# Optimization experiments

Measured on AMD Instinct MI355X. Metric: run time of the kernel, lower is better.

The kernel has to match this reference:

```python
import jax, jax.numpy as jnp
import numpy as np

N_HEAD = 32
N_KV_HEAD = 8
HEAD_DIM = 64
ROPE_THETA = 10000.0


def apply_rope(x):
    # x: [B, H, T, D], interleaved-pair RoPE (rotary_embedding_torch style)
    B, H, T, D = x.shape
    inv_freq = 1.0 / (ROPE_THETA ** (jnp.arange(0, D, 2, dtype=jnp.float32) / D))  # [D/2]
    ang = jnp.arange(T, dtype=jnp.float32)[:, None] * inv_freq[None, :]  # [T, D/2]
    cos = jnp.cos(ang)[None, None].astype(x.dtype)  # [1,1,T,D/2]
    sin = jnp.sin(ang)[None, None].astype(x.dtype)
    xe = x[..., 0::2]
    xo = x[..., 1::2]
    re = xe * cos - xo * sin
    ro = xo * cos + xe * sin
    return jnp.stack([re, ro], axis=-1).reshape(B, H, T, D)


def setup_inputs() -> dict:
    key = jax.random.key(0)
    ks = jax.random.split(key, 5)
    B, T, C = 2, 2048, 2048
    kv_dim = N_KV_HEAD * HEAD_DIM
    s = 0.02
    return {
        "x": jax.random.normal(ks[0], (B, T, C), jnp.float32),
        "wq": jax.random.normal(ks[1], (C, C), jnp.float32) * s,
        "wk": jax.random.normal(ks[2], (C, kv_dim), jnp.float32) * s,
        "wv": jax.random.normal(ks[3], (C, kv_dim), jnp.float32) * s,
        "wo": jax.random.normal(ks[4], (C, C), jnp.float32) * s,
    }


def reference(x, wq, wk, wv, wo):
    B, T, C = x.shape
    hd = HEAD_DIM
    q = (x @ wq).reshape(B, T, N_HEAD, hd).transpose(0, 2, 1, 3)      # [B,H,T,d]
    k = (x @ wk).reshape(B, T, N_KV_HEAD, hd).transpose(0, 2, 1, 3)   # [B,Hkv,T,d]
    v = (x @ wv).reshape(B, T, N_KV_HEAD, hd).transpose(0, 2, 1, 3)
    q = apply_rope(q)
    k = apply_rope(k)
    rep = N_HEAD // N_KV_HEAD
    k = jnp.repeat(k, rep, axis=1)  # repeat_interleave over head dim
    v = jnp.repeat(v, rep, axis=1)
    att = jnp.einsum('bhqd,bhkd->bhqk', q, k) * (1.0 / np.sqrt(hd))
    causal = jnp.tril(jnp.ones((T, T), dtype=bool))
    att = jnp.where(causal[None, None], att, jnp.finfo(att.dtype).min)
    att = jax.nn.softmax(att, axis=-1)
    y = jnp.einsum('bhqk,bhkd->bhqd', att, v)
    y = y.transpose(0, 2, 1, 3).reshape(B, T, C)
    return y @ wo
```

## Files before the change

kernel.cpp:

```cpp
#include <hip/hip_runtime.h>
#include <hip/hip_bf16.h>
#include <cstdint>
#include <cstddef>


using bf16 = __hip_bfloat16;
using f32x4  = __attribute__((ext_vector_type(4))) float;
using f32x16 = __attribute__((ext_vector_type(16))) float;
using short8 = __attribute__((ext_vector_type(8))) short;
using u32x4  = __attribute__((ext_vector_type(4))) unsigned int;

typedef __attribute__((address_space(1))) const void* gp1_t;
typedef __attribute__((address_space(3))) void*       lp3_t;

#define GLOAD_LDS16(g, l)                                                     \
  __builtin_amdgcn_global_load_lds((gp1_t)(const void*)(g), (lp3_t)(void*)(l), 16, 0, 0)

#define MFMA16(a, b, c) __builtin_amdgcn_mfma_f32_16x16x32_bf16(a, b, c, 0, 0, 0)
#define MFMA32(a, b, c) __builtin_amdgcn_mfma_f32_32x32x16_bf16(a, b, c, 0, 0, 0)

static constexpr int Bd  = 2;
static constexpr int Td  = 2048;
static constexpr int Cd  = 2048;
static constexpr int NH  = 32;
static constexpr int NKV = 8;
static constexpr int HD  = 64;
static constexpr int Md  = Bd * Td;

__device__ inline float bf2f(unsigned short u) {
  union { unsigned int i; float f; } v; v.i = ((unsigned int)u) << 16; return v.f;
}
__device__ inline unsigned short f2bfbits(float f) {
  union { float f; unsigned int u; } v; v.f = f;
  unsigned int r = v.u + 0x7fffu + ((v.u >> 16) & 1u);
  return (unsigned short)(r >> 16);
}
__device__ inline unsigned int pkbf(float a, float b) {
  unsigned int r;
  asm("v_cvt_pk_bf16_f32 %0, %1, %2" : "=v"(r) : "v"(a), "v"(b));
  return r;
}
__device__ inline void plswapf(float& a, float& b) {
  asm("v_permlane32_swap_b32 %0, %1" : "+v"(a), "+v"(b));
}
__device__ inline void plswapu(unsigned int& a, unsigned int& b) {
  asm("v_permlane32_swap_b32 %0, %1" : "+v"(a), "+v"(b));
}
__device__ inline float hmax16(const f32x16& v) {
  float a0 = fmaxf(v[0], v[1]),   a1 = fmaxf(v[2], v[3]);
  float a2 = fmaxf(v[4], v[5]),   a3 = fmaxf(v[6], v[7]);
  float a4 = fmaxf(v[8], v[9]),   a5 = fmaxf(v[10], v[11]);
  float a6 = fmaxf(v[12], v[13]), a7 = fmaxf(v[14], v[15]);
  float b0 = fmaxf(a0, a1), b1 = fmaxf(a2, a3);
  float b2 = fmaxf(a4, a5), b3 = fmaxf(a6, a7);
  return fmaxf(fmaxf(b0, b1), fmaxf(b2, b3));
}
__device__ inline float hsum16(const f32x16& v) {
  float a0 = v[0]+v[1],   a1 = v[2]+v[3],   a2 = v[4]+v[5],   a3 = v[6]+v[7];
  float a4 = v[8]+v[9],   a5 = v[10]+v[11], a6 = v[12]+v[13], a7 = v[14]+v[15];
  float b0 = a0+a1, b1 = a2+a3, b2 = a4+a5, b3 = a6+a7;
  return (b0+b1)+(b2+b3);
}

__global__ __launch_bounds__(256) void prep1_kernel(const float* __restrict__ x,
                                                    const float* __restrict__ wq,
                                                    const float* __restrict__ wk,
                                                    const float* __restrict__ wv,
                                                    const float* __restrict__ wo,
                                                    bf16* __restrict__ xb,
                                                    bf16* __restrict__ w1,
                                                    bf16* __restrict__ woT) {
  __shared__ float tile[32][33];
  int bid = blockIdx.x, tid = threadIdx.x;
  if (bid < 8192) {
    int i = bid * 256 + tid;
    float4 v = ((const float4*)x)[i];
    ushort4 o;
    o.x = f2bfbits(v.x); o.y = f2bfbits(v.y); o.z = f2bfbits(v.z); o.w = f2bfbits(v.w);
    ((ushort4*)xb)[i] = o;
    return;
  }
  const float* in; bf16* out; int Cc, bx, by;
  if (bid < 12288)      { int l = bid - 8192;  in = wq; out = w1;                        Cc = 2048; bx = l & 63; by = l >> 6; }
  else if (bid < 13312) { int l = bid - 12288; in = wk; out = w1 + (size_t)2048 * 2048;  Cc = 512;  bx = l & 15; by = l >> 4; }
  else if (bid < 14336) { int l = bid - 13312; in = wv; out = w1 + (size_t)2560 * 2048;  Cc = 512;  bx = l & 15; by = l >> 4; }
  else                  { int l = bid - 14336; in = wo; out = woT;                       Cc = 2048; bx = l & 63; by = l >> 6; }
  int tx = tid & 31, ty = tid >> 5;
  int col = bx * 32 + tx;
#pragma unroll
  for (int i = 0; i < 4; ++i) {
    int row = by * 32 + ty + i * 8;
    tile[ty + i * 8][tx] = in[(size_t)row * Cc + col];
  }
  __syncthreads();
#pragma unroll
  for (int i = 0; i < 4; ++i) {
    int orow = bx * 32 + ty + i * 8;
    int ocol = by * 32 + tx;
    out[(size_t)orow * 2048 + ocol] = __float2bfloat16(tile[tx][ty + i * 8]);
  }
}

__global__ __launch_bounds__(256) void transpose_f2b(const float* __restrict__ in,
                                                     bf16* __restrict__ out,
                                                     int R, int Cc) {
  __shared__ float tile[32][33];
  int tx = threadIdx.x & 31, ty = threadIdx.x >> 5;
  int bx = blockIdx.x, by = blockIdx.y;
  int col = bx * 32 + tx;
#pragma unroll
  for (int i = 0; i < 4; ++i) {
    int row = by * 32 + ty + i * 8;
    tile[ty + i * 8][tx] = in[(size_t)row * Cc + col];
  }
  __syncthreads();
#pragma unroll
  for (int i = 0; i < 4; ++i) {
    int orow = bx * 32 + ty + i * 8;
    int ocol = by * 32 + tx;
    out[(size_t)orow * R + ocol] = __float2bfloat16(tile[tx][ty + i * 8]);
  }
}

__global__ __launch_bounds__(512, 2) void gemm_qkv(const bf16* __restrict__ A,
                                                   const bf16* __restrict__ Bt,
                                                   void* __restrict__ Cp,
                                                   int M, int N, int K) {
  __shared__ __align__(16) char lds[114688];
  int tid = threadIdx.x;
  int w = tid >> 6, lane = tid & 63;
  int lr = lane & 15, lg = lane >> 4;
  int m0 = blockIdx.x * 256, n0 = blockIdx.y * 192;
  int wr = w >> 2, wc = w & 3;
  f32x4 acc[8][3] = {};

  size_t Kb = (size_t)K * 2;
  int c8 = lane & 7, r8 = lane >> 3;
  const char* Asrc = (const char*)A + (size_t)(m0 + w * 8 + r8) * Kb + ((c8 ^ r8) << 4);
  const char* Bsrc = (const char*)Bt + (size_t)(n0 + w * 8 + r8) * Kb + ((c8 ^ r8) << 4);
  char* AldsW = lds + w * 1024;
  char* BldsW = lds + 65536 + w * 1024;

#define GSTAGE(kt, bb) do {                                                   \
    _Pragma("unroll")                                                         \
    for (int j = 0; j < 4; ++j)                                               \
      GLOAD_LDS16(Asrc + (size_t)j * 64 * Kb + (size_t)(kt) * 2,              \
                  AldsW + (bb) * 32768 + j * 8192);                           \
    _Pragma("unroll")                                                         \
    for (int j = 0; j < 3; ++j)                                               \
      GLOAD_LDS16(Bsrc + (size_t)j * 64 * Kb + (size_t)(kt) * 2,              \
                  BldsW + (bb) * 24576 + j * 8192);                           \
  } while (0)

  int nkt = K >> 6;
  GSTAGE(0, 0);
  asm volatile("s_waitcnt vmcnt(0)" ::: "memory");
  __builtin_amdgcn_s_barrier();

  for (int t = 0; t < nkt; ++t) {
    int cur = t & 1;
    const char* Ab = lds + cur * 32768;
    const char* Bb = lds + 65536 + cur * 24576;
    short8 af[4][2], bfr[3][2];

    if (t + 1 < nkt) GSTAGE((t + 1) << 6, cur ^ 1);
#pragma unroll
    for (int kk = 0; kk < 2; ++kk) {
      int cb = (((kk << 2) | lg) ^ (lr & 7)) << 4;
#pragma unroll
      for (int f = 0; f < 4; ++f)
        af[f][kk] = *(const short8*)(Ab + (size_t)(wr * 128 + f * 16 + lr) * 128 + cb);
#pragma unroll
      for (int g = 0; g < 3; ++g)
        bfr[g][kk] = *(const short8*)(Bb + (size_t)(wc * 48 + g * 16 + lr) * 128 + cb);
    }
    __builtin_amdgcn_s_barrier();
    asm volatile("s_waitcnt lgkmcnt(0)" ::: "memory");
    __builtin_amdgcn_sched_barrier(0);
    __builtin_amdgcn_s_setprio(1);
#pragma unroll
    for (int f = 0; f < 4; ++f)
#pragma unroll
      for (int g = 0; g < 3; ++g)
#pragma unroll
        for (int kk = 0; kk < 2; ++kk)
          acc[f][g] = MFMA16(af[f][kk], bfr[g][kk], acc[f][g]);
    __builtin_amdgcn_s_setprio(0);
    __builtin_amdgcn_sched_barrier(0);
    __builtin_amdgcn_s_barrier();

#pragma unroll
    for (int kk = 0; kk < 2; ++kk) {
      int cb = (((kk << 2) | lg) ^ (lr & 7)) << 4;
#pragma unroll
      for (int f = 0; f < 4; ++f)
        af[f][kk] = *(const short8*)(Ab + (size_t)(wr * 128 + 64 + f * 16 + lr) * 128 + cb);
    }
    __builtin_amdgcn_s_barrier();
    asm volatile("s_waitcnt lgkmcnt(0)" ::: "memory");
    __builtin_amdgcn_sched_barrier(0);
    __builtin_amdgcn_s_setprio(1);
#pragma unroll
    for (int f = 0; f < 4; ++f)
#pragma unroll
      for (int g = 0; g < 3; ++g)
#pragma unroll
        for (int kk = 0; kk < 2; ++kk)
          acc[4 + f][g] = MFMA16(af[f][kk], bfr[g][kk], acc[4 + f][g]);
    __builtin_amdgcn_s_setprio(0);
    __builtin_amdgcn_sched_barrier(0);
    asm volatile("s_waitcnt vmcnt(0)" ::: "memory");
    __builtin_amdgcn_s_barrier();
  }
#undef GSTAGE

  bf16* Qb  = (bf16*)Cp;
  bf16* Kb2 = Qb + (size_t)Bd * NH * Td * HD;
  bf16* Vtb = Kb2 + (size_t)Bd * NKV * Td * HD;

  int b    = m0 >> 11;
  int col0 = n0 + wc * 48;

  if (col0 >= 2560) {
    int tg = (m0 & 2047) + wr * 128;
    int d0 = col0 - 2560;
    char* tb = lds + w * 14336;
#pragma unroll
    for (int i = 0; i < 8; ++i)
#pragma unroll
      for (int j = 0; j < 3; ++j)
#pragma unroll
        for (int r = 0; r < 4; r += 2) {
          int dl = j * 16 + lr;
          int tt = i * 16 + lg * 4 + r;
          unsigned int pk = pkbf(acc[i][j][r], acc[i][j][r + 1]);
          *(unsigned int*)(tb + (((size_t)dl * 256 + tt * 2) ^ ((dl & 7) << 4))) = pk;
        }
    asm volatile("s_waitcnt lgkmcnt(0)" ::: "memory");
    __builtin_amdgcn_sched_barrier(0);
#pragma unroll
    for (int p = 0; p < 12; ++p) {
      int c  = p * 64 + lane;
      int dl = c >> 4;
      int tc = c & 15;
      int dg = d0 + dl;
      int h  = dg >> 6, dd = dg & 63;
      u32x4 v = *(const u32x4*)(tb + (((size_t)dl * 256 + tc * 16) ^ ((dl & 7) << 4)));
      *(u32x4*)((char*)Vtb + ((((size_t)b * NKV + h) * 64 + dd) * Td + tg) * 2 + tc * 16) = v;
    }
    return;
  }

  const float RC  = -0.41524101186092029f;
  const float QSC = 0.18033688011112042f;
  int odd = lane & 1;
#pragma unroll
  for (int j = 0; j < 3; ++j) {
    int ncol = col0 + j * 16 + lr;
    int d  = ncol & 63;
    float inv = __builtin_amdgcn_exp2f((float)(d >> 1) * RC);
#pragma unroll
    for (int i = 0; i < 8; ++i) {
#pragma unroll
      for (int r = 0; r < 4; ++r) {
        int mrow = m0 + wr * 128 + i * 16 + lg * 4 + r;
        int t = mrow & 2047;
        float raw = acc[i][j][r];
        float p = __shfl_xor(raw, 1);
        float rev = (float)t * inv * 0.15915494309189535f;
        rev = rev - floorf(rev);
        float s = __builtin_amdgcn_sinf(rev);
        float c = __builtin_amdgcn_cosf(rev);
        float res = odd ? (raw * c + p * s) : (raw * c - p * s);
        if (ncol < 2048) {
          int h = ncol >> 6;
          Qb[(((size_t)b * NH + h) * Td + t) * HD + d] = __float2bfloat16(res * QSC);
        } else if (ncol < 2560) {
          int h = (ncol - 2048) >> 6;
          Kb2[(((size_t)b * NKV + h) * Td + t) * HD + d] = __float2bfloat16(res);
        } else {
          int dg = ncol - 2560;
          int h = dg >> 6, dd = dg & 63;
          Vtb[(((size_t)b * NKV + h) * 64 + dd) * Td + t] = __float2bfloat16(raw);
        }
      }
    }
  }
}

__global__ __launch_bounds__(512, 2) void gemm_out(const bf16* __restrict__ A,
                                                   const bf16* __restrict__ Bt,
                                                   float* __restrict__ Cp,
                                                   int M, int N, int K) {
  __shared__ __align__(16) char lds[98304];
  int tid = threadIdx.x;
  int w = tid >> 6, lane = tid & 63;
  int lr = lane & 15, lg = lane >> 4;
  int m0 = blockIdx.x * 256, n0 = blockIdx.y * 128;
  int wr = w >> 2, wc = w & 3;
  f32x4 acc[8][2] = {};

  size_t Kb = (size_t)K * 2;
  int c8 = lane & 7, r8 = lane >> 3;
  const char* Asrc = (const char*)A + (size_t)(m0 + w * 8 + r8) * Kb + ((c8 ^ r8) << 4);
  const char* Bsrc = (const char*)Bt + (size_t)(n0 + w * 8 + r8) * Kb + ((c8 ^ r8) << 4);
  char* AldsW = lds + w * 1024;
  char* BldsW = lds + 65536 + w * 1024;

#define GSTAGE(kt, bb) do {                                                   \
    _Pragma("unroll")                                                         \
    for (int j = 0; j < 4; ++j)                                               \
      GLOAD_LDS16(Asrc + (size_t)j * 64 * Kb + (size_t)(kt) * 2,              \
                  AldsW + (bb) * 32768 + j * 8192);                           \
    _Pragma("unroll")                                                         \
    for (int j = 0; j < 2; ++j)                                               \
      GLOAD_LDS16(Bsrc + (size_t)j * 64 * Kb + (size_t)(kt) * 2,              \
                  BldsW + (bb) * 16384 + j * 8192);                           \
  } while (0)

  int nkt = K >> 6;
  GSTAGE(0, 0);
  asm volatile("s_waitcnt vmcnt(0)" ::: "memory");
  __builtin_amdgcn_s_barrier();

  for (int t = 0; t < nkt; ++t) {
    int cur = t & 1;
    const char* Ab = lds + cur * 32768;
    const char* Bb = lds + 65536 + cur * 16384;
    short8 af[4][2], bfr[2][2];

    if (t + 1 < nkt) GSTAGE((t + 1) << 6, cur ^ 1);
#pragma unroll
    for (int kk = 0; kk < 2; ++kk) {
      int cb = (((kk << 2) | lg) ^ (lr & 7)) << 4;
#pragma unroll
      for (int f = 0; f < 4; ++f)
        af[f][kk] = *(const short8*)(Ab + (size_t)(wr * 128 + f * 16 + lr) * 128 + cb);
#pragma unroll
      for (int g = 0; g < 2; ++g)
        bfr[g][kk] = *(const short8*)(Bb + (size_t)(wc * 32 + g * 16 + lr) * 128 + cb);
    }
    __builtin_amdgcn_s_barrier();
    asm volatile("s_waitcnt lgkmcnt(0)" ::: "memory");
    __builtin_amdgcn_sched_barrier(0);
    __builtin_amdgcn_s_setprio(1);
#pragma unroll
    for (int f = 0; f < 4; ++f)
#pragma unroll
      for (int g = 0; g < 2; ++g)
#pragma unroll
        for (int kk = 0; kk < 2; ++kk)
          acc[f][g] = MFMA16(af[f][kk], bfr[g][kk], acc[f][g]);
    __builtin_amdgcn_s_setprio(0);
    __builtin_amdgcn_sched_barrier(0);
    __builtin_amdgcn_s_barrier();

#pragma unroll
    for (int kk = 0; kk < 2; ++kk) {
      int cb = (((kk << 2) | lg) ^ (lr & 7)) << 4;
#pragma unroll
      for (int f = 0; f < 4; ++f)
        af[f][kk] = *(const short8*)(Ab + (size_t)(wr * 128 + 64 + f * 16 + lr) * 128 + cb);
    }
    __builtin_amdgcn_s_barrier();
    asm volatile("s_waitcnt lgkmcnt(0)" ::: "memory");
    __builtin_amdgcn_sched_barrier(0);
    __builtin_amdgcn_s_setprio(1);
#pragma unroll
    for (int f = 0; f < 4; ++f)
#pragma unroll
      for (int g = 0; g < 2; ++g)
#pragma unroll
        for (int kk = 0; kk < 2; ++kk)
          acc[4 + f][g] = MFMA16(af[f][kk], bfr[g][kk], acc[4 + f][g]);
    __builtin_amdgcn_s_setprio(0);
    __builtin_amdgcn_sched_barrier(0);
    asm volatile("s_waitcnt vmcnt(0)" ::: "memory");
    __builtin_amdgcn_s_barrier();
  }
#undef GSTAGE

#pragma unroll
  for (int i = 0; i < 8; ++i)
#pragma unroll
    for (int j = 0; j < 2; ++j)
#pragma unroll
      for (int r = 0; r < 4; ++r) {
        int mrow = m0 + wr * 128 + i * 16 + lg * 4 + r;
        int ncol = n0 + wc * 32 + j * 16 + lr;
        Cp[(size_t)mrow * N + ncol] = acc[i][j][r];
      }
}

__global__ __launch_bounds__(512, 4) void attn_kernel(const bf16* __restrict__ Q,
                                                      const bf16* __restrict__ K,
                                                      const bf16* __restrict__ Vt,
                                                      bf16* __restrict__ Y) {
  __shared__ __align__(16) char lds[2 * 16384];
  int tid = threadIdx.x, w = tid >> 6, lane = tid & 63;
  int lq = lane & 31;
  int H  = lane >> 5;
  int qb = 7 - (int)blockIdx.y;
  int bh = blockIdx.x;
  int b = bh >> 5, h = bh & 31, kvh = h >> 2;
  int q0w = qb * 256 + w * 32;
  int qg  = q0w + lq;
  int tmax = qb * 4 + (w >> 1);
  int Nt   = qb * 4 + 4;

  const bf16* Qp = Q + (((size_t)b * NH + h) * Td) * HD;
  const char* Kg = (const char*)(K + (((size_t)b * NKV + kvh) * Td) * HD);
  const char* Vg = (const char*)(Vt + (((size_t)b * NKV + kvh) * HD) * Td);

  short8 qf[4];
#pragma unroll
  for (int ck = 0; ck < 4; ++ck)
    qf[ck] = *(const short8*)(Qp + (size_t)qg * HD + ck * 16 + H * 8);

  int srow   = lane >> 3;
  int scol16 = ((lane & 7) ^ srow) << 4;
  const char* Ksrc0 = Kg + (size_t)(w * 8 + srow) * 128 + scol16;
  const char* Vsrc0 = Vg + (size_t)(w * 8 + srow) * 4096 + scol16;
  char* KldsW[2] = { lds + w * 1024,          lds + 16384 + w * 1024 };
  char* VldsW[2] = { lds + 8192 + w * 1024,   lds + 24576 + w * 1024 };

#define STAGE_KV(tt, bb) do {                                                 \
    GLOAD_LDS16(Ksrc0 + (size_t)(tt) * 64 * 128, KldsW[bb]);                  \
    GLOAD_LDS16(Vsrc0 + (size_t)(tt) * 128,      VldsW[bb]);                  \
  } while (0)

  f32x16 acc0 = {}, acc1 = {};
  float m = -3e38f, l = 0.0f;
  int swz = (lq & 7) << 4;
  int rb0 = lq * 128, rb1 = (32 + lq) * 128;

  STAGE_KV(0, 0);
  asm volatile("s_waitcnt vmcnt(0)" ::: "memory");
  __syncthreads();

  for (int t = 0; t < Nt; ++t) {
    int cur = t & 1;
    if (t + 1 < Nt) STAGE_KV(t + 1, cur ^ 1);
    if (t <= tmax) {
      const char* Kl = lds + cur * 16384;
      const char* Vl = Kl + 8192;
      f32x16 s0 = {}, s1 = {};
      __builtin_amdgcn_s_setprio(1);
#pragma unroll
      for (int ck = 0; ck < 4; ++ck) {
        int c = (H * 16 + ck * 32) ^ swz;
        short8 kf0 = *(const short8*)(Kl + rb0 + c);
        short8 kf1 = *(const short8*)(Kl + rb1 + c);
        s0 = MFMA32(kf0, qf[ck], s0);
        s1 = MFMA32(kf1, qf[ck], s1);
      }
      __builtin_amdgcn_s_setprio(0);
      if (t == tmax) {
        int kvb = t * 64;
#pragma unroll
        for (int rr = 0; rr < 16; ++rr) {
          int krel = (rr & 3) + 8 * (rr >> 2) + 4 * H;
          if (kvb + krel > qg)      s0[rr] = -3e38f;
          if (kvb + 32 + krel > qg) s1[rr] = -3e38f;
        }
      }
      float mx = fmaxf(hmax16(s0), hmax16(s1));
      {
        float mb = mx;
        asm("" : "+v"(mb));
        plswapf(mx, mb);
        mx = fmaxf(mx, mb);
      }
      if (__any(mx > m + 8.0f)) {
        float mn = fmaxf(m, mx);
        float al = __builtin_amdgcn_exp2f(m - mn);
        m = mn;
        l *= al;
#pragma unroll
        for (int rr = 0; rr < 16; ++rr) { acc0[rr] *= al; acc1[rr] *= al; }
      }
#pragma unroll
      for (int rr = 0; rr < 16; ++rr) {
        s0[rr] = __builtin_amdgcn_exp2f(s0[rr] - m);
        s1[rr] = __builtin_amdgcn_exp2f(s1[rr] - m);
      }
      float ps = hsum16(s0) + hsum16(s1);
      {
        float pb = ps;
        asm("" : "+v"(pb));
        plswapf(ps, pb);
        ps += pb;
      }
      l += ps;
      short8 pf[4];
#pragma unroll
      for (int tt = 0; tt < 2; ++tt) {
        const f32x16& sv = tt ? s1 : s0;
#pragma unroll
        for (int a2 = 0; a2 < 2; ++a2) {
          unsigned int A0 = pkbf(sv[8*a2 + 0], sv[8*a2 + 1]);
          unsigned int A1 = pkbf(sv[8*a2 + 2], sv[8*a2 + 3]);
          unsigned int B0 = pkbf(sv[8*a2 + 4], sv[8*a2 + 5]);
          unsigned int B1 = pkbf(sv[8*a2 + 6], sv[8*a2 + 7]);
          plswapu(A0, B0);
          plswapu(A1, B1);
          u32x4 t4;
          t4[0] = A0; t4[1] = A1; t4[2] = B0; t4[3] = B1;
          pf[2*tt + a2] = __builtin_bit_cast(short8, t4);
        }
      }
      __builtin_amdgcn_s_setprio(1);
#pragma unroll
      for (int ks = 0; ks < 4; ++ks) {
        int c = (H * 16 + ks * 32) ^ swz;
        short8 vf0 = *(const short8*)(Vl + rb0 + c);
        short8 vf1 = *(const short8*)(Vl + rb1 + c);
        acc0 = MFMA32(vf0, pf[ks], acc0);
        acc1 = MFMA32(vf1, pf[ks], acc1);
      }
      __builtin_amdgcn_s_setprio(0);
    }
    asm volatile("s_waitcnt vmcnt(0)" ::: "memory");
    __syncthreads();
  }
#undef STAGE_KV

  float rn = 1.0f / l;
  bf16* Yp = Y + ((size_t)b * Td + qg) * Cd + h * HD;
#pragma unroll
  for (int rr = 0; rr < 16; rr += 2) {
    int d = (rr & 3) + 8 * (rr >> 2) + 4 * H;
    unsigned int w0 = pkbf(acc0[rr] * rn, acc0[rr + 1] * rn);
    unsigned int w1 = pkbf(acc1[rr] * rn, acc1[rr + 1] * rn);
    *(unsigned int*)(Yp + d)      = w0;
    *(unsigned int*)(Yp + 32 + d) = w1;
  }
}

extern "C" void kernel_launch(void* const* d_in, const int* in_sizes, int n_in,
                              void* d_out, int out_size, void* d_ws, size_t ws_size,
                              hipStream_t stream) {
  const float* x  = (const float*)d_in[0];
  const float* wq = (const float*)d_in[1];
  const float* wk = (const float*)d_in[2];
  const float* wv = (const float*)d_in[3];
  const float* wo = (const float*)d_in[4];

  char* ws = (char*)d_ws;
  const size_t o_xb  = 0;
  const size_t o_w1  = o_xb + (size_t)Md * Cd * 2;
  const size_t o_Q   = o_w1 + (size_t)3072 * Cd * 2;
  const size_t o_K   = o_Q + (size_t)Bd * NH * Td * HD * 2;
  const size_t o_V   = o_K + (size_t)Bd * NKV * Td * HD * 2;
  const size_t o_woT = o_V + (size_t)Bd * NKV * HD * Td * 2;
  const size_t need  = o_woT + (size_t)Cd * Cd * 2;

  bf16* xb  = (bf16*)(ws + o_xb);
  bf16* w1  = (bf16*)(ws + o_w1);
  bf16* Qb  = (bf16*)(ws + o_Q);
  bf16* Kb  = (bf16*)(ws + o_K);
  bf16* Vtb = (bf16*)(ws + o_V);
  bf16* yb  = xb;

  bool fused = (ws_size >= need);
  bf16* woT = fused ? (bf16*)(ws + o_woT) : w1;

  prep1_kernel<<<dim3(fused ? 18432 : 14336), dim3(256), 0, stream>>>(
      x, wq, wk, wv, wo, xb, w1, woT);
  gemm_qkv<<<dim3(Md / 256, 3072 / 192), dim3(512), 0, stream>>>(xb, w1, Qb, Md, 3072, Cd);
  if (!fused)
    transpose_f2b<<<dim3(Cd / 32, Cd / 32), dim3(256), 0, stream>>>(wo, w1, Cd, Cd);
  attn_kernel<<<dim3(Bd * NH, 8), dim3(512), 0, stream>>>(Qb, Kb, Vtb, yb);
  gemm_out<<<dim3(Md / 256, Cd / 128), dim3(512), 0, stream>>>(yb, woT, (float*)d_out, Md, Cd, Cd);
}
```

Baseline: 183.4 us.

## Switch QKV and output GEMMs to 4-stage K=32 pipelined LDS ring

Both GEMM kernels drop the double-buffered K=64 tiles and use a four-slot ring of K=32 tiles. Three stages are prefetched ahead with global-to-LDS loads, and partial vmcnt waits replace full drains. The per-iteration LDS reads become a single pass with one barrier instead of two half-passes with several barriers, so memory latency should overlap better with MFMA work. In exchange, the QKV kernel grows to 128KB of LDS, which may cut occupancy, and the shorter K steps mean more loop iterations and barriers in total.

```diff
diff --git a/kernel.cpp b/kernel.cpp
--- a/kernel.cpp
+++ b/kernel.cpp
@@ -126,7 +126,7 @@
                                                    const bf16* __restrict__ Bt,
                                                    void* __restrict__ Cp,
                                                    int M, int N, int K) {
-  __shared__ __align__(16) char lds[114688];
+  __shared__ __align__(16) char lds[131072];
   int tid = threadIdx.x;
   int w = tid >> 6, lane = tid & 63;
   int lr = lane & 15, lg = lane >> 4;
@@ -135,81 +135,51 @@
   f32x4 acc[8][3] = {};
 
   size_t Kb = (size_t)K * 2;
-  int c8 = lane & 7, r8 = lane >> 3;
-  const char* Asrc = (const char*)A + (size_t)(m0 + w * 8 + r8) * Kb + ((c8 ^ r8) << 4);
-  const char* Bsrc = (const char*)Bt + (size_t)(n0 + w * 8 + r8) * Kb + ((c8 ^ r8) << 4);
-  char* AldsW = lds + w * 1024;
-  char* BldsW = lds + 65536 + w * 1024;
-
-#define GSTAGE(kt, bb) do {                                                   \
-    _Pragma("unroll")                                                         \
-    for (int j = 0; j < 4; ++j)                                               \
-      GLOAD_LDS16(Asrc + (size_t)j * 64 * Kb + (size_t)(kt) * 2,              \
-                  AldsW + (bb) * 32768 + j * 8192);                           \
-    _Pragma("unroll")                                                         \
-    for (int j = 0; j < 3; ++j)                                               \
-      GLOAD_LDS16(Bsrc + (size_t)j * 64 * Kb + (size_t)(kt) * 2,              \
-                  BldsW + (bb) * 24576 + j * 8192);                           \
+  int srw = lane >> 2;
+  int swc = ((lane & 3) ^ (srw & 3)) << 4;
+  const char* AsrcT = (const char*)A + (size_t)(m0 + w * 16 + srw) * Kb + swc;
+  const char* BsrcT = (const char*)Bt + (size_t)(n0 + w * 16 + srw) * Kb + swc;
+  char* AldW = lds + w * 1024;
+  char* BldW = lds + 65536 + w * 1024;
+
+#define GSTAGE(ht) do {                                                       \
+    int _b = (ht) & 3; size_t _k = (size_t)(ht) * 64;                         \
+    GLOAD_LDS16(AsrcT + _k,                      AldW + _b * 16384);          \
+    GLOAD_LDS16(AsrcT + (size_t)128 * Kb + _k,   AldW + _b * 16384 + 8192);   \
+    GLOAD_LDS16(BsrcT + _k,                      BldW + _b * 16384);          \
+    GLOAD_LDS16(BsrcT + (size_t)128 * Kb + _k,   BldW + _b * 16384 + 8192);   \
   } while (0)
 
-  int nkt = K >> 6;
-  GSTAGE(0, 0);
-  asm volatile("s_waitcnt vmcnt(0)" ::: "memory");
+  int nht = K >> 5;
+  GSTAGE(0); GSTAGE(1); GSTAGE(2);
+  asm volatile("s_waitcnt vmcnt(8)" ::: "memory");
   __builtin_amdgcn_s_barrier();
 
-  for (int t = 0; t < nkt; ++t) {
-    int cur = t & 1;
-    const char* Ab = lds + cur * 32768;
-    const char* Bb = lds + 65536 + cur * 24576;
-    short8 af[4][2], bfr[3][2];
-
-    if (t + 1 < nkt) GSTAGE((t + 1) << 6, cur ^ 1);
-#pragma unroll
-    for (int kk = 0; kk < 2; ++kk) {
-      int cb = (((kk << 2) | lg) ^ (lr & 7)) << 4;
-#pragma unroll
-      for (int f = 0; f < 4; ++f)
-        af[f][kk] = *(const short8*)(Ab + (size_t)(wr * 128 + f * 16 + lr) * 128 + cb);
+  int cbase = (lg ^ (lr & 3)) << 4;
+  for (int ht = 0; ht < nht; ++ht) {
+    int buf = ht & 3;
+    if (ht + 3 < nht) GSTAGE(ht + 3);
+    const char* Ab = lds + buf * 16384;
+    const char* Bb = lds + 65536 + buf * 16384;
+    short8 af[8], bfr[3];
+#pragma unroll
+    for (int f = 0; f < 8; ++f)
+      af[f] = *(const short8*)(Ab + (size_t)(wr * 128 + f * 16 + lr) * 64 + cbase);
+#pragma unroll
+    for (int g = 0; g < 3; ++g)
+      bfr[g] = *(const short8*)(Bb + (size_t)(wc * 48 + g * 16 + lr) * 64 + cbase);
+    __builtin_amdgcn_s_setprio(1);
+#pragma unroll
+    for (int f = 0; f < 8; ++f)
 #pragma unroll
       for (int g = 0; g < 3; ++g)
-        bfr[g][kk] = *(const short8*)(Bb + (size_t)(wc * 48 + g * 16 + lr) * 128 + cb);
-    }
-    __builtin_amdgcn_s_barrier();
+        acc[f][g] = MFMA16(af[f], bfr[g], acc[f][g]);
+    __builtin_amdgcn_s_setprio(0);
     asm volatile("s_waitcnt lgkmcnt(0)" ::: "memory");
-    __builtin_amdgcn_sched_barrier(0);
-    __builtin_amdgcn_s_setprio(1);
-#pragma unroll
-    for (int f = 0; f < 4; ++f)
-#pragma unroll
-      for (int g = 0; g < 3; ++g)
-#pragma unroll
-        for (int kk = 0; kk < 2; ++kk)
-          acc[f][g] = MFMA16(af[f][kk], bfr[g][kk], acc[f][g]);
-    __builtin_amdgcn_s_setprio(0);
-    __builtin_amdgcn_sched_barrier(0);
-    __builtin_amdgcn_s_barrier();
-
-#pragma unroll
-    for (int kk = 0; kk < 2; ++kk) {
-      int cb = (((kk << 2) | lg) ^ (lr & 7)) << 4;
-#pragma unroll
-      for (int f = 0; f < 4; ++f)
-        af[f][kk] = *(const short8*)(Ab + (size_t)(wr * 128 + 64 + f * 16 + lr) * 128 + cb);
-    }
-    __builtin_amdgcn_s_barrier();
-    asm volatile("s_waitcnt lgkmcnt(0)" ::: "memory");
-    __builtin_amdgcn_sched_barrier(0);
-    __builtin_amdgcn_s_setprio(1);
-#pragma unroll
-    for (int f = 0; f < 4; ++f)
-#pragma unroll
-      for (int g = 0; g < 3; ++g)
-#pragma unroll
-        for (int kk = 0; kk < 2; ++kk)
-          acc[4 + f][g] = MFMA16(af[f][kk], bfr[g][kk], acc[4 + f][g]);
-    __builtin_amdgcn_s_setprio(0);
-    __builtin_amdgcn_sched_barrier(0);
-    asm volatile("s_waitcnt vmcnt(0)" ::: "memory");
+    if (ht + 3 < nht)
+      asm volatile("s_waitcnt vmcnt(8)" ::: "memory");
+    else
+      asm volatile("s_waitcnt vmcnt(0)" ::: "memory");
     __builtin_amdgcn_s_barrier();
   }
 #undef GSTAGE
@@ -301,81 +271,50 @@
   f32x4 acc[8][2] = {};
 
   size_t Kb = (size_t)K * 2;
-  int c8 = lane & 7, r8 = lane >> 3;
-  const char* Asrc = (const char*)A + (size_t)(m0 + w * 8 + r8) * Kb + ((c8 ^ r8) << 4);
-  const char* Bsrc = (const char*)Bt + (size_t)(n0 + w * 8 + r8) * Kb + ((c8 ^ r8) << 4);
-  char* AldsW = lds + w * 1024;
-  char* BldsW = lds + 65536 + w * 1024;
-
-#define GSTAGE(kt, bb) do {                                                   \
-    _Pragma("unroll")                                                         \
-    for (int j = 0; j < 4; ++j)                                               \
-      GLOAD_LDS16(Asrc + (size_t)j * 64 * Kb + (size_t)(kt) * 2,              \
-                  AldsW + (bb) * 32768 + j * 8192);                           \
-    _Pragma("unroll")                                                         \
-    for (int j = 0; j < 2; ++j)                                               \
-      GLOAD_LDS16(Bsrc + (size_t)j * 64 * Kb + (size_t)(kt) * 2,              \
-                  BldsW + (bb) * 16384 + j * 8192);                           \
+  int srw = lane >> 2;
+  int swc = ((lane & 3) ^ (srw & 3)) << 4;
+  const char* AsrcT = (const char*)A + (size_t)(m0 + w * 16 + srw) * Kb + swc;
+  const char* BsrcT = (const char*)Bt + (size_t)(n0 + w * 16 + srw) * Kb + swc;
+  char* AldW = lds + w * 1024;
+  char* BldW = lds + 65536 + w * 1024;
+
+#define GSTAGE(ht) do {                                                       \
+    int _b = (ht) & 3; size_t _k = (size_t)(ht) * 64;                         \
+    GLOAD_LDS16(AsrcT + _k,                      AldW + _b * 16384);          \
+    GLOAD_LDS16(AsrcT + (size_t)128 * Kb + _k,   AldW + _b * 16384 + 8192);   \
+    GLOAD_LDS16(BsrcT + _k,                      BldW + _b * 8192);           \
   } while (0)
 
-  int nkt = K >> 6;
-  GSTAGE(0, 0);
-  asm volatile("s_waitcnt vmcnt(0)" ::: "memory");
+  int nht = K >> 5;
+  GSTAGE(0); GSTAGE(1); GSTAGE(2);
+  asm volatile("s_waitcnt vmcnt(6)" ::: "memory");
   __builtin_amdgcn_s_barrier();
 
-  for (int t = 0; t < nkt; ++t) {
-    int cur = t & 1;
-    const char* Ab = lds + cur * 32768;
-    const char* Bb = lds + 65536 + cur * 16384;
-    short8 af[4][2], bfr[2][2];
-
-    if (t + 1 < nkt) GSTAGE((t + 1) << 6, cur ^ 1);
-#pragma unroll
-    for (int kk = 0; kk < 2; ++kk) {
-      int cb = (((kk << 2) | lg) ^ (lr & 7)) << 4;
-#pragma unroll
-      for (int f = 0; f < 4; ++f)
-        af[f][kk] = *(const short8*)(Ab + (size_t)(wr * 128 + f * 16 + lr) * 128 + cb);
+  int cbase = (lg ^ (lr & 3)) << 4;
+  for (int ht = 0; ht < nht; ++ht) {
+    int buf = ht & 3;
+    if (ht + 3 < nht) GSTAGE(ht + 3);
+    const char* Ab = lds + buf * 16384;
+    const char* Bb = lds + 65536 + buf * 8192;
+    short8 af[8], bfr[2];
+#pragma unroll
+    for (int f = 0; f < 8; ++f)
+      af[f] = *(const short8*)(Ab + (size_t)(wr * 128 + f * 16 + lr) * 64 + cbase);
+#pragma unroll
+    for (int g = 0; g < 2; ++g)
+      bfr[g] = *(const short8*)(Bb + (size_t)(wc * 32 + g * 16 + lr) * 64 + cbase);
+    __builtin_amdgcn_s_setprio(1);
+#pragma unroll
+    for (int f = 0; f < 8; ++f)
 #pragma unroll
       for (int g = 0; g < 2; ++g)
-        bfr[g][kk] = *(const short8*)(Bb + (size_t)(wc * 32 + g * 16 + lr) * 128 + cb);
-    }
-    __builtin_amdgcn_s_barrier();
+        acc[f][g] = MFMA16(af[f], bfr[g], acc[f][g]);
+    __builtin_amdgcn_s_setprio(0);
     asm volatile("s_waitcnt lgkmcnt(0)" ::: "memory");
-    __builtin_amdgcn_sched_barrier(0);
-    __builtin_amdgcn_s_setprio(1);
-#pragma unroll
-    for (int f = 0; f < 4; ++f)
-#pragma unroll
-      for (int g = 0; g < 2; ++g)
-#pragma unroll
-        for (int kk = 0; kk < 2; ++kk)
-          acc[f][g] = MFMA16(af[f][kk], bfr[g][kk], acc[f][g]);
-    __builtin_amdgcn_s_setprio(0);
-    __builtin_amdgcn_sched_barrier(0);
-    __builtin_amdgcn_s_barrier();
-
-#pragma unroll
-    for (int kk = 0; kk < 2; ++kk) {
-      int cb = (((kk << 2) | lg) ^ (lr & 7)) << 4;
-#pragma unroll
-      for (int f = 0; f < 4; ++f)
-        af[f][kk] = *(const short8*)(Ab + (size_t)(wr * 128 + 64 + f * 16 + lr) * 128 + cb);
-    }
-    __builtin_amdgcn_s_barrier();
-    asm volatile("s_waitcnt lgkmcnt(0)" ::: "memory");
-    __builtin_amdgcn_sched_barrier(0);
-    __builtin_amdgcn_s_setprio(1);
-#pragma unroll
-    for (int f = 0; f < 4; ++f)
-#pragma unroll
-      for (int g = 0; g < 2; ++g)
-#pragma unroll
-        for (int kk = 0; kk < 2; ++kk)
-          acc[4 + f][g] = MFMA16(af[f][kk], bfr[g][kk], acc[4 + f][g]);
-    __builtin_amdgcn_s_setprio(0);
-    __builtin_amdgcn_sched_barrier(0);
-    asm volatile("s_waitcnt vmcnt(0)" ::: "memory");
+    if (ht + 3 < nht)
+      asm volatile("s_waitcnt vmcnt(6)" ::: "memory");
+    else
+      asm volatile("s_waitcnt vmcnt(0)" ::: "memory");
     __builtin_amdgcn_s_barrier();
   }
 #undef GSTAGE
```

New measurement: 193.0 us. 5.2% more time.
